# Kernel tuning notes

Hardware: AMD Instinct MI355X
Metric: run time of the kernel (lower is better)

## Reference

```python
import jax, jax.numpy as jnp
import numpy as np

N, B, C_IN, C, E = 50000, 2, 64, 64, 800000


def _xavier(k, shape):
    bound = np.sqrt(6.0 / (shape[0] + shape[1]))
    return jax.random.uniform(k, shape, jnp.float32, -bound, bound)


def setup_inputs() -> dict:
    key = jax.random.key(0)
    ks = jax.random.split(key, 12)
    X = jax.random.normal(ks[0], (N, B, C_IN), jnp.float32)
    edge_index = jax.random.randint(ks[1], (2, E), 0, N, jnp.int64)
    edge_weight = jax.random.uniform(ks[2], (E,), jnp.float32)
    weight_n = _xavier(ks[3], (C_IN, C))
    weight_e = _xavier(ks[4], (1, C))
    query_w = _xavier(ks[5], (C, C))
    key_w = _xavier(ks[6], (C, C))
    # nn.Linear(3C, 1): store transposed weight [3C, 1] and bias [1]
    lb = 1.0 / np.sqrt(3 * C)
    att_w = jax.random.uniform(ks[7], (3 * C, 1), jnp.float32, -lb, lb)
    att_b = jax.random.uniform(ks[8], (1,), jnp.float32, -lb, lb)
    # nn.Linear(2C, C): store transposed weight [2C, C] and bias [C]
    lb2 = 1.0 / np.sqrt(2 * C)
    out_w = jax.random.uniform(ks[9], (2 * C, C), jnp.float32, -lb2, lb2)
    out_b = jax.random.uniform(ks[10], (C,), jnp.float32, -lb2, lb2)
    return {
        "X": X, "edge_index": edge_index, "edge_weight": edge_weight,
        "weight_n": weight_n, "weight_e": weight_e,
        "query_w": query_w, "key_w": key_w,
        "att_w": att_w, "att_b": att_b,
        "out_w": out_w, "out_b": out_b,
    }


def reference(X, edge_index, edge_weight, weight_n, weight_e,
              query_w, key_w, att_w, att_b, out_w, out_b):
    # node projection: [N, B, C]
    x = jnp.einsum('nbi,ic->nbc', X, weight_n)
    src, dst = edge_index[0], edge_index[1]  # x_j = x[src], x_i = x[dst]
    # edge embedding: [E, C]
    edge_emb = edge_weight[:, None] * weight_e[0][None, :]

    x_j = x[src]  # [E, B, C]
    x_i = x[dst]  # [E, B, C]
    q = jnp.einsum('ebc,cd->ebd', x_j, query_w)
    k = jnp.einsum('ebc,cd->ebd', x_i, key_w)
    # linear_att on concat([q, k, edge_emb]) == split matmul (avoids [E,B,3C] concat)
    wq, wk, we = att_w[:C], att_w[C:2 * C], att_w[2 * C:]
    att_logit = (q @ wq) + (k @ wk) + (edge_emb @ we)[:, None, :] + att_b  # [E, B, 1]
    att = jax.nn.sigmoid(att_logit)
    gate = jax.nn.sigmoid(edge_emb)[:, None, :]  # [E, 1, C]
    msg = att * x_j * gate  # [E, B, C]

    aggr = jax.ops.segment_sum(msg, dst, num_segments=N)  # [N, B, C]

    # linear_out(cat([x, aggr])) as split matmul
    upd = (jnp.einsum('nbc,cd->nbd', x, out_w[:C])
           + jnp.einsum('nbc,cd->nbd', aggr, out_w[C:]) + out_b)
    return x + upd
```

## Files before the change

### kernel.cpp

```cpp
#include <hip/hip_runtime.h>

#define NN 50000
#define BB 2
#define CC 64
#define EE 800000
#define RR (NN * BB)
#define CAP 48
#define K1BLK (RR / 32)
#define K4BLK (EE / 256)

typedef float f4_t __attribute__((ext_vector_type(4)));
typedef float f2_t __attribute__((ext_vector_type(2)));

#define LOG2E 1.44269504f

__device__ __forceinline__ float fsig_(float x) {
    return __builtin_amdgcn_rcpf(1.0f + __builtin_amdgcn_exp2f(x * -LOG2E));
}

__device__ __forceinline__ float bcast_(float v, int d) {
    return __uint_as_float(__builtin_amdgcn_readlane(__float_as_uint(v), d));
}

__global__ void k0_prep(const float* __restrict__ qw, const float* __restrict__ kw,
                        const float* __restrict__ we, const float* __restrict__ aw,
                        const float* __restrict__ wn, const float* __restrict__ ow,
                        float* __restrict__ prep, float* __restrict__ Wc) {
    int t = threadIdx.x;
    if (blockIdx.x == 0) {
        __shared__ float qv_s[64], kv_s[64];
        if (t < 64) {
            float sq = 0.f, sk = 0.f;
            for (int d = 0; d < 64; ++d) {
                sq = fmaf(qw[t * 64 + d], aw[d], sq);
                sk = fmaf(kw[t * 64 + d], aw[64 + d], sk);
            }
            qv_s[t] = sq; kv_s[t] = sk;
            prep[t] = sq; prep[64 + t] = sk;
            prep[320 + t] = -we[t] * LOG2E;
        }
        if (t == 128) {
            float se = 0.f;
            for (int i = 0; i < 64; ++i) se = fmaf(we[i], aw[128 + i], se);
            prep[128] = se;
        }
        __syncthreads();
        if (t < 64) {
            float s = 0.f;
            for (int c = 0; c < 64; ++c) s = fmaf(wn[t * 64 + c], qv_s[c], s);
            prep[192 + t] = s;
        } else if (t < 128) {
            int d = t - 64;
            float s = 0.f;
            for (int c = 0; c < 64; ++c) s = fmaf(wn[d * 64 + c], kv_s[c], s);
            prep[256 + d] = s;
        }
    } else {
        int idx = (blockIdx.x - 1) * 256 + t;
        int d = idx >> 6, c = idx & 63;
        float s = wn[d * 64 + c];
        for (int k = 0; k < 64; ++k) s = fmaf(wn[d * 64 + k], ow[k * 64 + c], s);
        Wc[idx] = s;
    }
}

__global__ void __launch_bounds__(256) k1_node(
        const float* __restrict__ X, const float* __restrict__ wn,
        const float* __restrict__ Wc, const float* __restrict__ out_b,
        const float* __restrict__ prep,
        float* __restrict__ x2f, float* __restrict__ y0,
        float* __restrict__ dq, float* __restrict__ dk) {
    int wave = (blockIdx.x * 256 + threadIdx.x) >> 6;
    int lane = threadIdx.x & 63;
    int r0 = wave * 8;
    if (r0 >= RR) return;

    float xin[8];
    #pragma unroll
    for (int j = 0; j < 8; ++j) xin[j] = X[(r0 + j) * 64 + lane];

    float nq_l = prep[192 + lane];
    float nk_l = prep[256 + lane];

    float accx[8], accy[8];
    #pragma unroll
    for (int j = 0; j < 8; ++j) { accx[j] = 0.f; accy[j] = 0.f; }

    #pragma unroll 16
    for (int d = 0; d < 64; ++d) {
        float w0 = wn[d * 64 + lane];
        float wc = Wc[d * 64 + lane];
        #pragma unroll
        for (int j = 0; j < 8; ++j) {
            float s = bcast_(xin[j], d);
            accx[j] = fmaf(s, w0, accx[j]);
            accy[j] = fmaf(s, wc, accy[j]);
        }
    }

    float ob = out_b[lane];
    #pragma unroll
    for (int j = 0; j < 8; ++j) {
        int r = r0 + j;
        y0[r * 64 + lane] = accy[j] + ob;
        x2f[((r >> 1) * 64 + lane) * 2 + (r & 1)] = accx[j];
        float pq = xin[j] * nq_l;
        float pk = xin[j] * nk_l;
        #pragma unroll
        for (int o = 32; o > 0; o >>= 1) {
            pq += __shfl_xor(pq, o, 64);
            pk += __shfl_xor(pk, o, 64);
        }
        if (lane == j) { dq[r] = pq; dk[r] = pk; }
    }
}

__global__ void k4_scatter(const int* __restrict__ ei, const float* __restrict__ ew,
                           const float2* __restrict__ dq2, const float2* __restrict__ dk2,
                           const float* __restrict__ prep, const float* __restrict__ att_b,
                           int* __restrict__ cursor, f4_t* __restrict__ csr) {
    int e = blockIdx.x * blockDim.x + threadIdx.x;
    if (e >= EE) return;
    int src = ei[e], dst = ei[EE + e];
    float w = ew[e];
    float2 q = dq2[src];
    float2 k = dk2[dst];
    float esc = fmaf(w, prep[128], att_b[0]);
    float a0 = fsig_(q.x + k.x + esc);
    float a1 = fsig_(q.y + k.y + esc);
    int pos = atomicAdd(&cursor[dst], 1);
    if (pos < CAP) {
        f4_t rec = { __int_as_float(src * 64), w, a0, a1 };
        csr[dst * CAP + pos] = rec;
    }
}

__global__ void __launch_bounds__(256) k5_aggr(
        const int* __restrict__ cursor, const f4_t* __restrict__ csr,
        const f2_t* __restrict__ x2, const float* __restrict__ prep,
        float* __restrict__ aggr) {
    int n = (blockIdx.x * 256 + threadIdx.x) >> 6;
    int lane = threadIdx.x & 63;
    if (n >= NN) return;

    float weL = prep[320 + lane];
    int cnt = __builtin_amdgcn_readfirstlane(cursor[n]);
    cnt = cnt < CAP ? cnt : CAP;
    const f4_t* cp = csr + (size_t)n * CAP;

    float a0 = 0.f, a1 = 0.f;
    int i = 0;
    for (; i + 4 <= cnt; i += 4) {
        f4_t c0 = cp[i + 0];
        f4_t c1 = cp[i + 1];
        f4_t c2 = cp[i + 2];
        f4_t c3 = cp[i + 3];
        f2_t v0 = x2[__float_as_int(c0.x) + lane];
        f2_t v1 = x2[__float_as_int(c1.x) + lane];
        f2_t v2 = x2[__float_as_int(c2.x) + lane];
        f2_t v3 = x2[__float_as_int(c3.x) + lane];
        float g0 = __builtin_amdgcn_rcpf(1.0f + __builtin_amdgcn_exp2f(c0.y * weL));
        float g1 = __builtin_amdgcn_rcpf(1.0f + __builtin_amdgcn_exp2f(c1.y * weL));
        float g2 = __builtin_amdgcn_rcpf(1.0f + __builtin_amdgcn_exp2f(c2.y * weL));
        float g3 = __builtin_amdgcn_rcpf(1.0f + __builtin_amdgcn_exp2f(c3.y * weL));
        a0 = fmaf(c0.z * g0, v0.x, a0);  a1 = fmaf(c0.w * g0, v0.y, a1);
        a0 = fmaf(c1.z * g1, v1.x, a0);  a1 = fmaf(c1.w * g1, v1.y, a1);
        a0 = fmaf(c2.z * g2, v2.x, a0);  a1 = fmaf(c2.w * g2, v2.y, a1);
        a0 = fmaf(c3.z * g3, v3.x, a0);  a1 = fmaf(c3.w * g3, v3.y, a1);
    }
    for (; i < cnt; ++i) {
        f4_t c0 = cp[i];
        f2_t v0 = x2[__float_as_int(c0.x) + lane];
        float g0 = __builtin_amdgcn_rcpf(1.0f + __builtin_amdgcn_exp2f(c0.y * weL));
        a0 = fmaf(c0.z * g0, v0.x, a0);
        a1 = fmaf(c0.w * g0, v0.y, a1);
    }

    __builtin_nontemporal_store(a0, &aggr[(2 * n) * 64 + lane]);
    __builtin_nontemporal_store(a1, &aggr[(2 * n + 1) * 64 + lane]);
}

__global__ void __launch_bounds__(256) k6_out(
        const float* __restrict__ aggr, const float* __restrict__ y0,
        const float* __restrict__ ow, float* __restrict__ out) {
    int wave = (blockIdx.x * 256 + threadIdx.x) >> 6;
    int lane = threadIdx.x & 63;
    int r0 = wave * 8;
    if (r0 >= RR) return;

    float ain[8], acc[8];
    #pragma unroll
    for (int j = 0; j < 8; ++j) {
        ain[j] = __builtin_nontemporal_load(&aggr[(r0 + j) * 64 + lane]);
        acc[j] = __builtin_nontemporal_load(&y0[(r0 + j) * 64 + lane]);
    }

    #pragma unroll 16
    for (int d = 0; d < 64; ++d) {
        float w = ow[4096 + d * 64 + lane];
        #pragma unroll
        for (int j = 0; j < 8; ++j)
            acc[j] = fmaf(bcast_(ain[j], d), w, acc[j]);
    }

    #pragma unroll
    for (int j = 0; j < 8; ++j)
        __builtin_nontemporal_store(acc[j], &out[(r0 + j) * 64 + lane]);
}

extern "C" void kernel_launch(void* const* d_in, const int* in_sizes, int n_in,
                              void* d_out, int out_size, void* d_ws, size_t ws_size,
                              hipStream_t stream) {
    const float* X        = (const float*)d_in[0];
    const int*   ei       = (const int*)d_in[1];
    const float* ew       = (const float*)d_in[2];
    const float* weight_n = (const float*)d_in[3];
    const float* weight_e = (const float*)d_in[4];
    const float* query_w  = (const float*)d_in[5];
    const float* key_w    = (const float*)d_in[6];
    const float* att_w    = (const float*)d_in[7];
    const float* att_b    = (const float*)d_in[8];
    const float* out_w    = (const float*)d_in[9];
    const float* out_b    = (const float*)d_in[10];
    float* out = (float*)d_out;

    char* ws = (char*)d_ws;
    size_t off = 0;
    auto alloc = [&](size_t bytes) {
        char* p = ws + off;
        off += (bytes + 255) & ~(size_t)255;
        return p;
    };
    float*  x2f    = (float*)alloc(sizeof(float) * NN * CC * BB);
    float*  y0     = (float*)alloc(sizeof(float) * RR * CC);
    float*  aggr   = (float*)alloc(sizeof(float) * RR * CC);
    float*  dq     = (float*)alloc(sizeof(float) * RR);
    float*  dk     = (float*)alloc(sizeof(float) * RR);
    float*  prep   = (float*)alloc(sizeof(float) * 512);
    float*  Wc     = (float*)alloc(sizeof(float) * 4096);
    int*    cursor = (int*)alloc(sizeof(int) * NN);
    f4_t*   csr    = (f4_t*)alloc(sizeof(f4_t) * (size_t)NN * CAP);

    hipMemsetAsync(cursor, 0, sizeof(int) * NN, stream);

    hipLaunchKernelGGL(k0_prep, dim3(17), dim3(256), 0, stream,
                       query_w, key_w, weight_e, att_w, weight_n, out_w, prep, Wc);
    hipLaunchKernelGGL(k1_node, dim3(K1BLK), dim3(256), 0, stream,
                       X, weight_n, Wc, out_b, prep, x2f, y0, dq, dk);
    hipLaunchKernelGGL(k4_scatter, dim3(K4BLK), dim3(256), 0, stream,
                       ei, ew, (const float2*)dq, (const float2*)dk, prep, att_b,
                       cursor, csr);
    hipLaunchKernelGGL(k5_aggr, dim3(NN / 4), dim3(256), 0, stream,
                       cursor, csr, (const f2_t*)x2f, prep, aggr);
    hipLaunchKernelGGL(k6_out, dim3(RR / 32), dim3(256), 0, stream,
                       aggr, y0, out_w, out);
}
```

Measured before the change: 280.4 us.

## Fuse output projection into aggregation and shrink CSR records to 8 bytes

```diff
diff --git a/kernel.cpp b/kernel.cpp
--- a/kernel.cpp
+++ b/kernel.cpp
@@ -116,96 +116,90 @@
 }
 
 __global__ void k4_scatter(const int* __restrict__ ei, const float* __restrict__ ew,
-                           const float2* __restrict__ dq2, const float2* __restrict__ dk2,
-                           const float* __restrict__ prep, const float* __restrict__ att_b,
-                           int* __restrict__ cursor, f4_t* __restrict__ csr) {
+                           int* __restrict__ cursor, int2* __restrict__ csr) {
     int e = blockIdx.x * blockDim.x + threadIdx.x;
     if (e >= EE) return;
     int src = ei[e], dst = ei[EE + e];
     float w = ew[e];
-    float2 q = dq2[src];
-    float2 k = dk2[dst];
-    float esc = fmaf(w, prep[128], att_b[0]);
-    float a0 = fsig_(q.x + k.x + esc);
-    float a1 = fsig_(q.y + k.y + esc);
     int pos = atomicAdd(&cursor[dst], 1);
     if (pos < CAP) {
-        f4_t rec = { __int_as_float(src * 64), w, a0, a1 };
-        csr[dst * CAP + pos] = rec;
+        csr[dst * CAP + pos] = make_int2(src, __float_as_int(w));
     }
 }
 
 __global__ void __launch_bounds__(256) k5_aggr(
-        const int* __restrict__ cursor, const f4_t* __restrict__ csr,
-        const f2_t* __restrict__ x2, const float* __restrict__ prep,
-        float* __restrict__ aggr) {
+        const int* __restrict__ cursor, const int2* __restrict__ csr,
+        const f2_t* __restrict__ x2,
+        const float2* __restrict__ dq2, const float2* __restrict__ dk2,
+        const float* __restrict__ prep, const float* __restrict__ att_b,
+        const float* __restrict__ y0, const float* __restrict__ ow,
+        float* __restrict__ out) {
     int n = (blockIdx.x * 256 + threadIdx.x) >> 6;
     int lane = threadIdx.x & 63;
     if (n >= NN) return;
 
     float weL = prep[320 + lane];
+    float se  = prep[128];
+    float ab  = att_b[0];
+    float2 dkn = dk2[n];
+
     int cnt = __builtin_amdgcn_readfirstlane(cursor[n]);
     cnt = cnt < CAP ? cnt : CAP;
-    const f4_t* cp = csr + (size_t)n * CAP;
-
-    float a0 = 0.f, a1 = 0.f;
+    const int2* cp = csr + (size_t)n * CAP;
+
+    float acc0 = 0.f, acc1 = 0.f;
     int i = 0;
     for (; i + 4 <= cnt; i += 4) {
-        f4_t c0 = cp[i + 0];
-        f4_t c1 = cp[i + 1];
-        f4_t c2 = cp[i + 2];
-        f4_t c3 = cp[i + 3];
-        f2_t v0 = x2[__float_as_int(c0.x) + lane];
-        f2_t v1 = x2[__float_as_int(c1.x) + lane];
-        f2_t v2 = x2[__float_as_int(c2.x) + lane];
-        f2_t v3 = x2[__float_as_int(c3.x) + lane];
-        float g0 = __builtin_amdgcn_rcpf(1.0f + __builtin_amdgcn_exp2f(c0.y * weL));
-        float g1 = __builtin_amdgcn_rcpf(1.0f + __builtin_amdgcn_exp2f(c1.y * weL));
-        float g2 = __builtin_amdgcn_rcpf(1.0f + __builtin_amdgcn_exp2f(c2.y * weL));
-        float g3 = __builtin_amdgcn_rcpf(1.0f + __builtin_amdgcn_exp2f(c3.y * weL));
-        a0 = fmaf(c0.z * g0, v0.x, a0);  a1 = fmaf(c0.w * g0, v0.y, a1);
-        a0 = fmaf(c1.z * g1, v1.x, a0);  a1 = fmaf(c1.w * g1, v1.y, a1);
-        a0 = fmaf(c2.z * g2, v2.x, a0);  a1 = fmaf(c2.w * g2, v2.y, a1);
-        a0 = fmaf(c3.z * g3, v3.x, a0);  a1 = fmaf(c3.w * g3, v3.y, a1);
+        int2 r0 = cp[i + 0];
+        int2 r1 = cp[i + 1];
+        int2 r2 = cp[i + 2];
+        int2 r3 = cp[i + 3];
+        float2 q0 = dq2[r0.x];
+        float2 q1 = dq2[r1.x];
+        float2 q2 = dq2[r2.x];
+        float2 q3 = dq2[r3.x];
+        f2_t v0 = x2[(r0.x << 6) + lane];
+        f2_t v1 = x2[(r1.x << 6) + lane];
+        f2_t v2 = x2[(r2.x << 6) + lane];
+        f2_t v3 = x2[(r3.x << 6) + lane];
+        float w0 = __int_as_float(r0.y), w1 = __int_as_float(r1.y);
+        float w2 = __int_as_float(r2.y), w3 = __int_as_float(r3.y);
+        float e0 = fmaf(w0, se, ab), e1 = fmaf(w1, se, ab);
+        float e2 = fmaf(w2, se, ab), e3 = fmaf(w3, se, ab);
+        float g0 = __builtin_amdgcn_rcpf(1.0f + __builtin_amdgcn_exp2f(w0 * weL));
+        float g1 = __builtin_amdgcn_rcpf(1.0f + __builtin_amdgcn_exp2f(w1 * weL));
+        float g2 = __builtin_amdgcn_rcpf(1.0f + __builtin_amdgcn_exp2f(w2 * weL));
+        float g3 = __builtin_amdgcn_rcpf(1.0f + __builtin_amdgcn_exp2f(w3 * weL));
+        acc0 = fmaf(fsig_(q0.x + dkn.x + e0) * g0, v0.x, acc0);
+        acc1 = fmaf(fsig_(q0.y + dkn.y + e0) * g0, v0.y, acc1);
+        acc0 = fmaf(fsig_(q1.x + dkn.x + e1) * g1, v1.x, acc0);
+        acc1 = fmaf(fsig_(q1.y + dkn.y + e1) * g1, v1.y, acc1);
+        acc0 = fmaf(fsig_(q2.x + dkn.x + e2) * g2, v2.x, acc0);
+        acc1 = fmaf(fsig_(q2.y + dkn.y + e2) * g2, v2.y, acc1);
+        acc0 = fmaf(fsig_(q3.x + dkn.x + e3) * g3, v3.x, acc0);
+        acc1 = fmaf(fsig_(q3.y + dkn.y + e3) * g3, v3.y, acc1);
     }
     for (; i < cnt; ++i) {
-        f4_t c0 = cp[i];
-        f2_t v0 = x2[__float_as_int(c0.x) + lane];
-        float g0 = __builtin_amdgcn_rcpf(1.0f + __builtin_amdgcn_exp2f(c0.y * weL));
-        a0 = fmaf(c0.z * g0, v0.x, a0);
-        a1 = fmaf(c0.w * g0, v0.y, a1);
-    }
-
-    __builtin_nontemporal_store(a0, &aggr[(2 * n) * 64 + lane]);
-    __builtin_nontemporal_store(a1, &aggr[(2 * n + 1) * 64 + lane]);
-}
-
-__global__ void __launch_bounds__(256) k6_out(
-        const float* __restrict__ aggr, const float* __restrict__ y0,
-        const float* __restrict__ ow, float* __restrict__ out) {
-    int wave = (blockIdx.x * 256 + threadIdx.x) >> 6;
-    int lane = threadIdx.x & 63;
-    int r0 = wave * 8;
-    if (r0 >= RR) return;
-
-    float ain[8], acc[8];
-    #pragma unroll
-    for (int j = 0; j < 8; ++j) {
-        ain[j] = __builtin_nontemporal_load(&aggr[(r0 + j) * 64 + lane]);
-        acc[j] = __builtin_nontemporal_load(&y0[(r0 + j) * 64 + lane]);
-    }
-
+        int2 r0 = cp[i];
+        float2 q0 = dq2[r0.x];
+        f2_t v0 = x2[(r0.x << 6) + lane];
+        float w0 = __int_as_float(r0.y);
+        float e0 = fmaf(w0, se, ab);
+        float g0 = __builtin_amdgcn_rcpf(1.0f + __builtin_amdgcn_exp2f(w0 * weL));
+        acc0 = fmaf(fsig_(q0.x + dkn.x + e0) * g0, v0.x, acc0);
+        acc1 = fmaf(fsig_(q0.y + dkn.y + e0) * g0, v0.y, acc1);
+    }
+
+    float o0 = __builtin_nontemporal_load(&y0[(2 * n) * 64 + lane]);
+    float o1 = __builtin_nontemporal_load(&y0[(2 * n + 1) * 64 + lane]);
     #pragma unroll 16
     for (int d = 0; d < 64; ++d) {
         float w = ow[4096 + d * 64 + lane];
-        #pragma unroll
-        for (int j = 0; j < 8; ++j)
-            acc[j] = fmaf(bcast_(ain[j], d), w, acc[j]);
-    }
-
-    #pragma unroll
-    for (int j = 0; j < 8; ++j)
-        __builtin_nontemporal_store(acc[j], &out[(r0 + j) * 64 + lane]);
+        o0 = fmaf(bcast_(acc0, d), w, o0);
+        o1 = fmaf(bcast_(acc1, d), w, o1);
+    }
+    __builtin_nontemporal_store(o0, &out[(2 * n) * 64 + lane]);
+    __builtin_nontemporal_store(o1, &out[(2 * n + 1) * 64 + lane]);
 }
 
 extern "C" void kernel_launch(void* const* d_in, const int* in_sizes, int n_in,
@@ -233,13 +227,12 @@
     };
     float*  x2f    = (float*)alloc(sizeof(float) * NN * CC * BB);
     float*  y0     = (float*)alloc(sizeof(float) * RR * CC);
-    float*  aggr   = (float*)alloc(sizeof(float) * RR * CC);
     float*  dq     = (float*)alloc(sizeof(float) * RR);
     float*  dk     = (float*)alloc(sizeof(float) * RR);
     float*  prep   = (float*)alloc(sizeof(float) * 512);
     float*  Wc     = (float*)alloc(sizeof(float) * 4096);
     int*    cursor = (int*)alloc(sizeof(int) * NN);
-    f4_t*   csr    = (f4_t*)alloc(sizeof(f4_t) * (size_t)NN * CAP);
+    int2*   csr    = (int2*)alloc(sizeof(int2) * (size_t)NN * CAP);
 
     hipMemsetAsync(cursor, 0, sizeof(int) * NN, stream);
 
@@ -248,10 +241,9 @@
     hipLaunchKernelGGL(k1_node, dim3(K1BLK), dim3(256), 0, stream,
                        X, weight_n, Wc, out_b, prep, x2f, y0, dq, dk);
     hipLaunchKernelGGL(k4_scatter, dim3(K4BLK), dim3(256), 0, stream,
-                       ei, ew, (const float2*)dq, (const float2*)dk, prep, att_b,
-                       cursor, csr);
+                       ei, ew, cursor, csr);
     hipLaunchKernelGGL(k5_aggr, dim3(NN / 4), dim3(256), 0, stream,
-                       cursor, csr, (const f2_t*)x2f, prep, aggr);
-    hipLaunchKernelGGL(k6_out, dim3(RR / 32), dim3(256), 0, stream,
-                       aggr, y0, out_w, out);
-}
+                       cursor, csr, (const f2_t*)x2f,
+                       (const float2*)dq, (const float2*)dk, prep, att_b,
+                       y0, out_w, out);
+}
```

Result: no change. 277.0 us (-1.2%).
